# Kernel optimization log

Hardware: AMD Instinct MI355X
Metric: run time of the kernel (lower is better)

## Reference

```python
import math
import jax, jax.numpy as jnp
import numpy as np

# irreps layout (flat, e3nn ordering: all scalars first, then vectors as (mul,3)):
#   pseduo: 64x0e + 32x1o  -> dim 160, 96 irreps
#   edge:   32x0e + 32x1o  -> dim 128, 64 irreps
PS, PV = 64, 32
ES, EV = 32, 32
H, NB = 8, 16
N_NODES, N_EDGES = 8192, 65536
MSG_DIM = PS + 3 * PV           # msg_irreps = pseduo_irreps (default)
NIR = PS + PV                   # num_irreps of pseduo
SQRT3 = math.sqrt(3.0)

def _split(x, ns, nv):
    # flat spherical tensor -> (scalars [..,ns], vectors [..,nv,3])
    return x[..., :ns], x[..., ns:].reshape(x.shape[:-1] + (nv, 3))

def _o3_linear(s, v, Ws, Wv):
    # e3nn o3.Linear: independent channel mixing per l, fan-in normalized
    so = (s @ Ws) / math.sqrt(Ws.shape[0])
    vo = jnp.einsum('...ic,io->...oc', v, Wv) / math.sqrt(Wv.shape[0])
    return so, vo

def setup_inputs() -> dict:
    key = jax.random.key(0)
    k = jax.random.split(key, 20)
    f32 = jnp.float32
    return {
        'pseduo_x': jax.random.normal(k[0], (N_NODES, PS + 3 * PV), f32),
        'rbf': jax.random.normal(k[1], (N_EDGES, NB), f32),
        'rsh': jax.random.normal(k[2], (N_EDGES, ES + 3 * EV), f32),
        'edge_index': jax.random.randint(k[3], (2, N_EDGES), 0, N_NODES),
        'Wq_s': jax.random.normal(k[4], (PS, H * PS), f32),
        'Wq_v': jax.random.normal(k[5], (PV, H * PV), f32),
        'Wk_s': jax.random.normal(k[6], (2 * PS, H * PS), f32),
        'Wk_v': jax.random.normal(k[7], (2 * PV, H * PV), f32),
        'Wp_s': jax.random.normal(k[8], (2 * PS, ES), f32),
        'Wp_v': jax.random.normal(k[9], (2 * PV, EV), f32),
        'Wrbf': jax.random.normal(k[10], (NB, ES + EV), f32) / math.sqrt(NB),
        'Wv_s': jax.random.normal(k[11], (ES + EV, H * PS), f32),
        'Wv_v': jax.random.normal(k[12], (2 * EV, H * PV), f32),
        'Wm_s': jax.random.normal(k[13], (H * PS, PS), f32),
        'Wm_v': jax.random.normal(k[14], (H * PV, PV), f32),
        'ln_g': jnp.ones((NIR,), f32),
        'ln_b': jnp.zeros((NIR,), f32),
        'W1': jax.random.normal(k[15], (NIR, NIR), f32) / math.sqrt(NIR),
        'b1': jnp.zeros((NIR,), f32),
        'W2': jax.random.normal(k[16], (NIR, NIR), f32) / math.sqrt(NIR),
        'b2': jnp.zeros((NIR,), f32),
    }

def reference(pseduo_x, rbf, rsh, edge_index, Wq_s, Wq_v, Wk_s, Wk_v, Wp_s, Wp_v,
              Wrbf, Wv_s, Wv_v, Wm_s, Wm_v, ln_g, ln_b, W1, b1, W2, b2):
    src, dst = edge_index[0], edge_index[1]
    s, v = _split(pseduo_x, PS, PV)

    # pseduo_ij = cat([x_i, x_j]) -> irreps pseduo*2
    sij = jnp.concatenate([s[src], s[dst]], axis=-1)            # [E, 2*PS]
    vij = jnp.concatenate([v[src], v[dst]], axis=-2)            # [E, 2*PV, 3]

    # multi-head query (per node) and key (per edge)
    q_s, q_v = _o3_linear(s, v, Wq_s, Wq_v)
    q_s = q_s.reshape(-1, H, PS); q_v = q_v.reshape(-1, H, PV, 3)
    k_s, k_v = _o3_linear(sij, vij, Wk_s, Wk_v)
    k_s = k_s.reshape(-1, H, PS); k_v = k_v.reshape(-1, H, PV, 3)

    # edge filter: rsh_conv(rsh, rbf_lin(rbf))
    scal = rbf @ Wrbf                                           # [E, ES+EV]
    rs, rv = _split(rsh, ES, EV)
    e_s = rs * scal[:, :ES]
    e_v = rv * scal[:, ES:, None]

    # sph_ij = edge * pseduo_lin(pseduo_ij)   (elementwise on flat layout)
    p_s, p_v = _o3_linear(sij, vij, Wp_s, Wp_v)
    sph_s = e_s * p_s                                           # [E, ES]
    sph_v = e_v * p_v                                           # [E, EV, 3]

    # depthwise CG self-coupling x (x) x, filter {0e, 1o} -> 64x0e + 64x1o
    c0 = jnp.concatenate([sph_s * sph_s,
                          jnp.sum(sph_v * sph_v, axis=-1) / SQRT3], axis=-1)  # [E, 64]
    sv = sph_s[..., None] * sph_v                               # 0e x 1o -> 1o
    c1 = jnp.concatenate([sv, sv], axis=-2)                     # [E, 64, 3]

    val_s, val_v = _o3_linear(c0, c1, Wv_s, Wv_v)
    val_s = val_s.reshape(-1, H, PS); val_v = val_v.reshape(-1, H, PV, 3)

    # attention logits: (query[src] * key).sum over flat msg dim, per head
    proj = (jnp.einsum('ehd,ehd->eh', q_s[src], k_s) +
            jnp.einsum('ehdc,ehdc->eh', q_v[src], k_v))
    logits = proj / math.sqrt(MSG_DIM)

    # scatter-softmax over destination nodes
    m = jax.ops.segment_max(logits, dst, num_segments=N_NODES)
    ex = jnp.exp(logits - m[dst])
    den = jax.ops.segment_sum(ex, dst, num_segments=N_NODES)
    attn = ex / den[dst]                                        # [E, H]

    # scatter-aggregate messages to nodes
    msg_s = jax.ops.segment_sum(attn[..., None] * val_s, dst, num_segments=N_NODES)
    msg_v = jax.ops.segment_sum(attn[..., None, None] * val_v, dst, num_segments=N_NODES)

    m_s, m_v = _o3_linear(msg_s.reshape(-1, H * PS),
                          msg_v.reshape(-1, H * PV, 3), Wm_s, Wm_v)

    # NormGate: EvNorm (per-irrep norm, node LayerNorm) + 2-layer silu MLP gate
    n0 = jnp.concatenate([jnp.abs(m_s), jnp.linalg.norm(m_v, axis=-1)], axis=-1)  # [N, 96]
    mu = jnp.mean(n0, axis=-1, keepdims=True)
    var = jnp.var(n0, axis=-1, keepdims=True)
    x1 = (n0 - mu) / jnp.sqrt(var + 1e-5) * ln_g + ln_b
    inv = 1.0 / (n0 + 1e-6)                                    # 1 / (|h_l| + eps)
    g = jax.nn.silu(jax.nn.silu(x1 @ W1 + b1) @ W2 + b2)
    f = inv * g
    out_s = m_s * f[:, :PS]
    out_v = m_v * f[:, PS:, None]
    return jnp.concatenate([out_s, out_v.reshape(-1, 3 * PV)], axis=-1)
```

## Files before the change

kernel.cpp:

```cpp
#include <hip/hip_runtime.h>

typedef unsigned short u16;
typedef unsigned int u32;

#define NN 8192
#define NE 65536
#define INV160 0.07905694150420949f

__device__ __forceinline__ float BF(u16 u){ return __uint_as_float(((u32)u)<<16); }
__device__ __forceinline__ float LD(const void* p, u32 i, int f){
  return f ? ((const float*)p)[i] : BF(((const u16*)p)[i]);
}
__device__ __forceinline__ int LDI(const void* p, u32 i, int f64){
  return f64 ? (int)((const long long*)p)[i] : ((const int*)p)[i];
}

__global__ void k_detect(
    const void* b0, const void* b1, const void* b2, const void* b3,
    const void* b4, const void* b5, const void* b6, const void* b7,
    const void* b8, const void* b9, const void* b10, const void* b11,
    const void* b12, const void* b13, const void* b14, const void* b15,
    const void* b16, const void* b17, const void* b18, const void* b19,
    const void* b20, int* flags)
{
  const void* bufs[21] = {b0,b1,b2,b3,b4,b5,b6,b7,b8,b9,b10,
                          b11,b12,b13,b14,b15,b16,b17,b18,b19,b20};
  int i = threadIdx.x;
  if (i >= 21) return;
  const u32* w = (const u32*)bufs[i];
  if (i == 3){
    int allz = 1;
    for (int k=0;k<32;k++) if (w[2*k+1] != 0u) allz = 0;
    flags[3] = allz;
  } else {
    int cnt = 0;
    for (int k=0;k<40;k++){
      u32 lo = w[k] & 0xFFFFu;
      u32 e = (lo>>7)&0xFFu;
      if (e>=123u && e<=131u) cnt++;
    }
    flags[i] = (cnt>=20) ? 0 : 1;
  }
}

__global__ void k_sentinel(float* __restrict__ out, int n){
  int i = blockIdx.x*256+threadIdx.x;
  if (i<n) out[i] = 12345.0f;
}

__global__ __launch_bounds__(384) void k_prep4(
    const void* __restrict__ X, const void* __restrict__ Wq_s,
    const void* __restrict__ Wq_v, const void* __restrict__ Wk_s,
    const void* __restrict__ Wk_v, const int* __restrict__ flags,
    int hc0, float* __restrict__ qtab, float* __restrict__ kbtab,
    float* __restrict__ dotAA)
{
  __shared__ float xr[4][160];
  __shared__ float dsum[4][4];
  const int fX=flags[0], fqs=flags[4], fqv=flags[5], fks=flags[6], fkv=flags[7];
  const int fall = fqs & fqv & fks & fkv;
  const int t=threadIdx.x; const int n0=blockIdx.x*4;
  for(int u=t;u<640;u+=384){ int m=u/160,k=u-m*160; xr[m][k]=LD(X,(u32)(n0+m)*160+k,fX); }
  if (t<16) dsum[t>>2][t&3]=0.f;
  __syncthreads();
  if (t<256){
    const int o=hc0*64+t;
    float q[4]={0,0,0,0}, ka[4]={0,0,0,0}, kb[4]={0,0,0,0};
    if (fall){
      const float* wqs=(const float*)Wq_s;
      const float* wks=(const float*)Wk_s;
      for(int i=0;i<64;i++){
        float wq=wqs[(u32)i*512+o], wa=wks[(u32)i*512+o], wb=wks[(u32)(64+i)*512+o];
        #pragma unroll
        for(int m=0;m<4;m++){ float s=xr[m][i]; q[m]+=s*wq; ka[m]+=s*wa; kb[m]+=s*wb; }
      }
    } else {
      for(int i=0;i<64;i++){
        float wq=LD(Wq_s,(u32)i*512+o,fqs);
        float wa=LD(Wk_s,(u32)i*512+o,fks);
        float wb=LD(Wk_s,(u32)(64+i)*512+o,fks);
        #pragma unroll
        for(int m=0;m<4;m++){ float s=xr[m][i]; q[m]+=s*wq; ka[m]+=s*wa; kb[m]+=s*wb; }
      }
    }
    #pragma unroll
    for(int m=0;m<4;m++){
      float qs = q[m]*0.125f;
      float kas= ka[m]*0.08838834764831845f;
      float kbs= kb[m]*0.08838834764831845f;
      qtab [(u32)(n0+m)*640+t]=qs;
      kbtab[(u32)(n0+m)*640+t]=kbs;
      float d=qs*kas;
      for(int s2=1;s2<64;s2<<=1) d+=__shfl_xor(d,s2,64);
      if((t&63)==0) atomicAdd(&dsum[m][t>>6],d);
    }
  } else {
    const int ol=t-256;
    const int o=hc0*32+ol;
    float q[4][3]={}, ka[4][3]={}, kb[4][3]={};
    if (fall){
      const float* wqv=(const float*)Wq_v;
      const float* wkv=(const float*)Wk_v;
      for(int j=0;j<32;j++){
        float wq=wqv[(u32)j*256+o], wa=wkv[(u32)j*256+o], wb=wkv[(u32)(32+j)*256+o];
        #pragma unroll
        for(int m=0;m<4;m++){
          #pragma unroll
          for(int c=0;c<3;c++){
            float x=xr[m][64+j*3+c];
            q[m][c]+=x*wq; ka[m][c]+=x*wa; kb[m][c]+=x*wb;
          }
        }
      }
    } else {
      for(int j=0;j<32;j++){
        float wq=LD(Wq_v,(u32)j*256+o,fqv);
        float wa=LD(Wk_v,(u32)j*256+o,fkv);
        float wb=LD(Wk_v,(u32)(32+j)*256+o,fkv);
        #pragma unroll
        for(int m=0;m<4;m++){
          #pragma unroll
          for(int c=0;c<3;c++){
            float x=xr[m][64+j*3+c];
            q[m][c]+=x*wq; ka[m][c]+=x*wa; kb[m][c]+=x*wb;
          }
        }
      }
    }
    const float sq=0.17677669529663687f;
    const float sk=0.125f;
    #pragma unroll
    for(int m=0;m<4;m++){
      float d=0.f;
      u32 base=(u32)(n0+m)*640+256+(u32)ol*3;
      #pragma unroll
      for(int c=0;c<3;c++){
        float qs=q[m][c]*sq, kas=ka[m][c]*sk, kbs=kb[m][c]*sk;
        qtab[base+c]=qs; kbtab[base+c]=kbs;
        d+=qs*kas;
      }
      for(int s2=1;s2<32;s2<<=1) d+=__shfl_xor(d,s2,64);
      if((t&31)==0) atomicAdd(&dsum[m][ol>>5],d);
    }
  }
  __syncthreads();
  if (t<16){ int m=t>>2, hh=t&3; dotAA[(u32)(n0+m)*8+hc0+hh]=dsum[m][hh]; }
}

__global__ __launch_bounds__(512) void k_elog4(
    const void* __restrict__ ei, const int* __restrict__ flags,
    const float* __restrict__ qtab, const float* __restrict__ kbtab,
    const float* __restrict__ dotAA, const u32* __restrict__ elist,
    int hc0, float* __restrict__ logits)
{
  const int f64=flags[3];
  const int t=threadIdx.x;
  const int e=(int)elist[(u32)blockIdx.x*8+(t>>6)], l=t&63;
  const int src=LDI(ei,(u32)e,f64);
  const int dst=LDI(ei,(u32)NE+e,f64);
  const float4* q4=(const float4*)qtab + (u32)src*160;
  const float4* b4=(const float4*)kbtab + (u32)dst*160;
  float a0=0.f,a1=0.f,a2=0.f,a3=0.f;
  {
    float4 a=q4[l], b=b4[l];
    float d=a.x*b.x+a.y*b.y+a.z*b.z+a.w*b.w;
    int h=l>>4;
    a0+=(h==0)?d:0.f; a1+=(h==1)?d:0.f; a2+=(h==2)?d:0.f; a3+=(h==3)?d:0.f;
  }
  {
    float4 a=q4[64+l], b=b4[64+l];
    float d=a.x*b.x+a.y*b.y+a.z*b.z+a.w*b.w;
    int h=l/24;
    a0+=(h==0)?d:0.f; a1+=(h==1)?d:0.f; a2+=(h==2)?d:0.f;
  }
  if (l<32){
    float4 a=q4[128+l], b=b4[128+l];
    float d=a.x*b.x+a.y*b.y+a.z*b.z+a.w*b.w;
    a2+=(l<8)?d:0.f; a3+=(l>=8)?d:0.f;
  }
  for(int m=1;m<64;m<<=1){
    a0+=__shfl_xor(a0,m,64); a1+=__shfl_xor(a1,m,64);
    a2+=__shfl_xor(a2,m,64); a3+=__shfl_xor(a3,m,64);
  }
  if (l<4){
    float cr=(l==0)?a0:(l==1)?a1:(l==2)?a2:a3;
    logits[(u32)e*8+hc0+l]=(dotAA[(u32)src*8+hc0+l]+cr)*INV160;
  }
}

__global__ __launch_bounds__(256) void k_fold(
    const void* __restrict__ Wv_s, const void* __restrict__ Wv_v,
    const void* __restrict__ Wm_s, const void* __restrict__ Wm_v,
    const int* __restrict__ flags,
    float* __restrict__ Wfold, float* __restrict__ Vfold)
{
  const int fvs=flags[11], fvv=flags[12], fms=flags[13], fmv=flags[14];
  const int b=blockIdx.x, t=threadIdx.x;
  if (b<128){
    int idx=b*256+t;
    int i=idx>>6, o=idx&63;
    int h=i>>6, iin=i&63;
    float a=0.f;
    for(int d=0;d<64;d++)
      a += LD(Wv_s,(u32)iin*512 + h*64 + d, fvs) * LD(Wm_s,(u32)(h*64+d)*64 + o, fms);
    Wfold[idx]=a*0.0055242717280199026f;
  } else {
    int idx=(b-128)*256+t;
    int h=idx>>10, r=idx&1023, j2=r>>5, o2=r&31;
    float a=0.f;
    for(int dl=0;dl<32;dl++){
      int i2=h*32+dl;
      a += (LD(Wv_v,(u32)j2*256+i2,fvv)+LD(Wv_v,(u32)(32+j2)*256+i2,fvv))
           *LD(Wm_v,(u32)i2*32+o2,fmv);
    }
    Vfold[idx]=a*0.0078125f;
  }
}

__global__ __launch_bounds__(256) void k_pprep(
    const void* __restrict__ X, const void* __restrict__ Wp_s,
    const void* __restrict__ Wp_v, const int* __restrict__ flags,
    float* __restrict__ pA, float* __restrict__ pB)
{
  __shared__ float xr[160];
  const int fX=flags[0], fps=flags[8], fpv=flags[9];
  const int t=threadIdx.x, n=blockIdx.x;
  if (t<160) xr[t]=LD(X,(u32)n*160+t,fX);
  __syncthreads();
  if (t<64){
    const int j=t&31, half=t>>5;
    float a=0.f;
    if (fps){
      const float* wp=(const float*)Wp_s;
      for(int i=0;i<64;i++) a+=xr[i]*wp[(u32)(half*64+i)*32+j];
    } else {
      for(int i=0;i<64;i++) a+=xr[i]*LD(Wp_s,(u32)(half*64+i)*32+j,fps);
    }
    float* d_ = half? pB:pA;
    d_[(u32)n*128+j]=a*0.08838834764831845f;
  } else {
    const int idx=t-64;
    const int half=idx/96;
    const int r=idx-half*96;
    const int j=r/3, c=r-3*j;
    float a=0.f;
    if (fpv){
      const float* wp=(const float*)Wp_v;
      for(int k=0;k<32;k++) a+=xr[64+k*3+c]*wp[(u32)(half*32+k)*32+j];
    } else {
      for(int k=0;k<32;k++) a+=xr[64+k*3+c]*LD(Wp_v,(u32)(half*32+k)*32+j,fpv);
    }
    float* d_ = half? pB:pA;
    d_[(u32)n*128+32+j*3+c]=a*0.125f;
  }
}

__global__ __launch_bounds__(256) void k_count(
    const void* __restrict__ ei, const int* __restrict__ flags,
    u32* __restrict__ cnt)
{
  int e = blockIdx.x*256 + threadIdx.x;
  int dst = LDI(ei,(u32)NE+e,flags[3]);
  atomicAdd(&cnt[dst],1u);
}
__global__ __launch_bounds__(256) void k_scan(
    u32* __restrict__ cnt, u32* __restrict__ off, u32* __restrict__ cur)
{
  __shared__ u32 s[NN];
  __shared__ u32 tsum[256];
  const int t=threadIdx.x;
  for(int u=t;u<NN;u+=256) s[u]=cnt[u];
  __syncthreads();
  const u32 base=(u32)t*32;
  u32 sum=0;
  for(int k=0;k<32;k++) sum+=s[base+k];
  tsum[t]=sum;
  __syncthreads();
  if(t==0){
    u32 run=0;
    for(int i=0;i<256;i++){ u32 v=tsum[i]; tsum[i]=run; run+=v; }
  }
  __syncthreads();
  u32 run=tsum[t];
  for(int k=0;k<32;k++){
    u32 v=s[base+k];
    off[base+k]=run; cur[base+k]=run;
    run+=v;
  }
  if(t==255) off[NN]=run;
}
__global__ __launch_bounds__(256) void k_fill(
    const void* __restrict__ ei, const int* __restrict__ flags,
    u32* __restrict__ cur, u32* __restrict__ elist)
{
  int e = blockIdx.x*256 + threadIdx.x;
  int dst = LDI(ei,(u32)NE+e,flags[3]);
  u32 p = atomicAdd(&cur[dst],1u);
  elist[p] = (u32)e;
}

__global__ __launch_bounds__(256) void k_nodeval(
    const float* __restrict__ logits, const float* __restrict__ pA,
    const float* __restrict__ pBt,
    const u32* __restrict__ off, const u32* __restrict__ elist,
    const void* __restrict__ ei, const void* __restrict__ rbf,
    const void* __restrict__ rsh, const void* __restrict__ Wrbf,
    const float* __restrict__ Wfold, const float* __restrict__ Vfold,
    const void* __restrict__ ln_g, const void* __restrict__ ln_b,
    const void* __restrict__ W1, const void* __restrict__ b1,
    const void* __restrict__ W2, const void* __restrict__ b2,
    const int* __restrict__ flags, float* __restrict__ out)
{
  __shared__ float wrb[1024];
  __shared__ float pB[128];
  __shared__ float ubuf[8][160];
  __shared__ int   ebuf[8];
  __shared__ float ag[1280];
  __shared__ float partf[16][64];
  __shared__ float partv[192];
  __shared__ float mrow[160];
  __shared__ float n0[96], x1[96], y1[96], fl[96];
  const int frb=flags[1], frs=flags[2], f64=flags[3], fwr=flags[10];
  const int fg=flags[15], fbb=flags[16], f1=flags[17], fb1=flags[18];
  const int f2=flags[19], fb2=flags[20];
  const int fastg = frb & frs;
  const int fastt = fg & fbb & f1 & fb1 & f2 & fb2;
  const int t=threadIdx.x; const int n=blockIdx.x;
  for(int u=t;u<1024;u+=256) wrb[u]=LD(Wrbf,u,fwr);
  if (t<128) pB[t]=pBt[(u32)n*128+t];
  __syncthreads();

  const int h=t>>5, j=t&31;
  const u32 o0=off[n], o1=off[n+1];

  float mx=-3.4e38f;
  for(u32 p=o0+j; p<o1; p+=32) mx=fmaxf(mx, logits[(u32)elist[p]*8+h]);
  #pragma unroll
  for(int s2=1;s2<32;s2<<=1) mx=fmaxf(mx, __shfl_xor(mx,s2,64));
  float sm=0.f;
  for(u32 p=o0+j; p<o1; p+=32) sm+=__expf(logits[(u32)elist[p]*8+h]-mx);
  #pragma unroll
  for(int s2=1;s2<32;s2<<=1) sm+=__shfl_xor(sm,s2,64);
  const float winv=(sm>0.f)?1.f/sm:0.f;

  float a0=0.f,a1=0.f,a2=0.f,a3=0.f,a4=0.f;
  for (u32 base=o0; base<o1; base+=8){
    u32 rem=o1-base; int nb = rem<8u ? (int)rem : 8;
    if (h<nb){
      u32 e=elist[base+h];
      if (j==0) ebuf[h]=(int)e;
      int src=LDI(ei,e,f64);
      const float* pa=pA+(u32)src*128;
      float ps  = pa[j]        + pB[j];
      float pv0 = pa[32+j*3+0] + pB[32+j*3+0];
      float pv1 = pa[32+j*3+1] + pB[32+j*3+1];
      float pv2 = pa[32+j*3+2] + pB[32+j*3+2];
      float scs=0.f, scv=0.f;
      float rs0,rs1,rs2,rs3;
      if (fastg){
        const float* rb=(const float*)rbf + (size_t)e*16;
        #pragma unroll
        for(int r=0;r<16;r++){
          float x=rb[r];
          scs+=x*wrb[r*64+j]; scv+=x*wrb[r*64+32+j];
        }
        const float* rs=(const float*)rsh + (size_t)e*128;
        rs0=rs[j]; rs1=rs[32+j*3+0]; rs2=rs[32+j*3+1]; rs3=rs[32+j*3+2];
      } else {
        for(int r=0;r<16;r++){
          float x=LD(rbf,(u32)e*16+r,frb);
          scs+=x*wrb[r*64+j]; scv+=x*wrb[r*64+32+j];
        }
        rs0=LD(rsh,(u32)e*128+j,frs);
        rs1=LD(rsh,(u32)e*128+32+j*3+0,frs);
        rs2=LD(rsh,(u32)e*128+32+j*3+1,frs);
        rs3=LD(rsh,(u32)e*128+32+j*3+2,frs);
      }
      float ss = rs0 * scs * ps;
      float v0 = rs1 * scv * pv0;
      float v1 = rs2 * scv * pv1;
      float v2 = rs3 * scv * pv2;
      ubuf[h][j]        = ss*ss;
      ubuf[h][32+j]     = (v0*v0+v1*v1+v2*v2)*0.57735026918962576f;
      ubuf[h][64+3*j+0] = ss*v0;
      ubuf[h][64+3*j+1] = ss*v1;
      ubuf[h][64+3*j+2] = ss*v2;
    }
    __syncthreads();
    for(int q=0;q<nb;q++){
      float w=__expf(logits[(u32)ebuf[q]*8+h]-mx)*winv;
      a0+=w*ubuf[q][j];        a1+=w*ubuf[q][32+j];
      a2+=w*ubuf[q][64+3*j+0]; a3+=w*ubuf[q][64+3*j+1]; a4+=w*ubuf[q][64+3*j+2];
    }
    __syncthreads();
  }
  ag[h*64+j]=a0; ag[h*64+32+j]=a1;
  ag[512+h*96+3*j+0]=a2; ag[512+h*96+3*j+1]=a3; ag[512+h*96+3*j+2]=a4;
  __syncthreads();

  {
    const int o4=t&15, p=t>>4;
    const float4* Wf4=(const float4*)Wfold;
    float ax=0.f,ay=0.f,az=0.f,aw=0.f;
    const int i0=p*32;
    for(int i=i0;i<i0+32;i++){
      float a=ag[i];
      float4 wv=Wf4[(u32)i*16+o4];
      ax+=a*wv.x; ay+=a*wv.y; az+=a*wv.z; aw+=a*wv.w;
    }
    partf[p][o4*4+0]=ax; partf[p][o4*4+1]=ay;
    partf[p][o4*4+2]=az; partf[p][o4*4+3]=aw;
  }
  if (t<192){
    const int o2=t&31, c=(t>>5)%3, p=t/96;
    float a=0.f;
    for(int hh=p*4;hh<p*4+4;hh++)
      for(int j2=0;j2<32;j2++)
        a += ag[512+hh*96+j2*3+c]*Vfold[(u32)hh*1024+j2*32+o2];
    partv[t]=a;
  }
  __syncthreads();
  if (t<64){
    float s=0.f;
    #pragma unroll
    for(int p2=0;p2<16;p2++) s+=partf[p2][t];
    mrow[t]=s;
  } else if (t<160){
    int q=t-64;
    mrow[64+(q&31)*3+(q>>5)]=partv[q]+partv[q+96];
  }
  __syncthreads();

  if (t<96){
    float val;
    if (t<64) val=fabsf(mrow[t]);
    else { int o2=t-64;
      float a=mrow[64+o2*3],b=mrow[64+o2*3+1],c=mrow[64+o2*3+2];
      val=sqrtf(a*a+b*b+c*c); }
    n0[t]=val;
  }
  __syncthreads();
  float mu=0.f,ss2=0.f;
  for(int i=0;i<96;i++){ float v=n0[i]; mu+=v; ss2+=v*v; }
  mu*=(1.f/96.f);
  float var=fmaxf(ss2*(1.f/96.f)-mu*mu,0.f);
  float rstd=rsqrtf(var+1e-5f);
  if (t<96){
    float gv = fg  ? ((const float*)ln_g)[t] : LD(ln_g,t,fg);
    float bv = fbb ? ((const float*)ln_b)[t] : LD(ln_b,t,fbb);
    x1[t]=(n0[t]-mu)*rstd*gv+bv;
  }
  __syncthreads();
  if (t<96){
    float a = fb1 ? ((const float*)b1)[t] : LD(b1,t,fb1);
    if (fastt){
      const float* w1=(const float*)W1;
      for(int i=0;i<96;i++) a+=x1[i]*w1[(u32)i*96+t];
    } else {
      for(int i=0;i<96;i++) a+=x1[i]*LD(W1,i*96+t,f1);
    }
    y1[t]=a/(1.f+__expf(-a));
  }
  __syncthreads();
  if (t<96){
    float a = fb2 ? ((const float*)b2)[t] : LD(b2,t,fb2);
    if (fastt){
      const float* w2=(const float*)W2;
      for(int i=0;i<96;i++) a+=y1[i]*w2[(u32)i*96+t];
    } else {
      for(int i=0;i<96;i++) a+=y1[i]*LD(W2,i*96+t,f2);
    }
    float gg=a/(1.f+__expf(-a));
    fl[t]=gg/(n0[t]+1e-6f);
  }
  __syncthreads();
  if (t<160){
    float v;
    if (t<64) v=mrow[t]*fl[t];
    else { int q=t-64; int o2=q/3; v=mrow[t]*fl[64+o2]; }
    out[(u32)n*160+t]=v;
  }
}

extern "C" void kernel_launch(void* const* d_in, const int* in_sizes, int n_in,
                              void* d_out, int out_size, void* d_ws, size_t ws_size,
                              hipStream_t stream)
{
  (void)in_sizes; (void)n_in;
  const void* X    = d_in[0];
  const void* rbf  = d_in[1];
  const void* rsh  = d_in[2];
  const void* ei   = d_in[3];
  const void* Wq_s = d_in[4];
  const void* Wq_v = d_in[5];
  const void* Wk_s = d_in[6];
  const void* Wk_v = d_in[7];
  const void* Wp_s = d_in[8];
  const void* Wp_v = d_in[9];
  const void* Wrbf = d_in[10];
  const void* Wv_s = d_in[11];
  const void* Wv_v = d_in[12];
  const void* Wm_s = d_in[13];
  const void* Wm_v = d_in[14];
  const void* ln_g = d_in[15];
  const void* ln_b = d_in[16];
  const void* W1   = d_in[17];
  const void* b1   = d_in[18];
  const void* W2   = d_in[19];
  const void* b2   = d_in[20];

  char* w = (char*)d_ws;
  int* flags     = (int*)w;   w += 256;
  float* logits  = (float*)w; w += (size_t)NE*8*4;
  u32* imax      = (u32*)w;   w += (size_t)NN*8*4;
  float* den     = (float*)w; w += (size_t)NN*8*4;
  char* uni = w;              w += (size_t)NN*1280*4;
  float* qtab  = (float*)uni;
  float* kbtab = (float*)(uni + (size_t)NN*640*4);
  float* pA    = (float*)uni;
  float* pB    = (float*)(uni + (size_t)NN*128*4);
  u32* csr_off = imax;
  u32* csr_cur = imax + 12288;
  float* Wfold = (float*)((char*)imax + 98304);
  float* Vfold = (float*)((char*)imax + 229376);
  u32* elist   = (u32*)den;
  float* dotAA = (float*)d_out;
  size_t required = (size_t)(w - (char*)d_ws);

  if (ws_size < required){
    k_sentinel<<<(out_size+255)/256,256,0,stream>>>((float*)d_out, out_size);
    return;
  }

  k_detect<<<1,64,0,stream>>>(X,rbf,rsh,ei,Wq_s,Wq_v,Wk_s,Wk_v,Wp_s,Wp_v,
                              Wrbf,Wv_s,Wv_v,Wm_s,Wm_v,ln_g,ln_b,W1,b1,W2,b2,flags);
  k_fold<<<160,256,0,stream>>>(Wv_s,Wv_v,Wm_s,Wm_v,flags,Wfold,Vfold);
  hipMemsetAsync(imax, 0, (size_t)NN*4, stream);
  k_count<<<NE/256,256,0,stream>>>(ei,flags,imax);
  k_scan<<<1,256,0,stream>>>(imax,csr_off,csr_cur);
  k_fill<<<NE/256,256,0,stream>>>(ei,flags,csr_cur,elist);
  for (int c=0;c<2;c++){
    k_prep4<<<NN/4,384,0,stream>>>(X,Wq_s,Wq_v,Wk_s,Wk_v,flags,c*4,qtab,kbtab,dotAA);
    k_elog4<<<NE/8,512,0,stream>>>(ei,flags,qtab,kbtab,dotAA,elist,c*4,logits);
  }
  k_pprep<<<NN,256,0,stream>>>(X,Wp_s,Wp_v,flags,pA,pB);
  k_nodeval<<<NN,256,0,stream>>>(logits,pA,pB,csr_off,elist,ei,rbf,rsh,Wrbf,
                                 Wfold,Vfold,ln_g,ln_b,W1,b1,W2,b2,flags,(float*)d_out);
}
```

Measured before the change: 446.6 us.

## Process four nodes per block in k_nodeval to amortize weight reads

Result: faster. 428.6 us (-4.0%).

```diff
diff --git a/kernel.cpp b/kernel.cpp
--- a/kernel.cpp
+++ b/kernel.cpp
@@ -311,174 +311,224 @@
     const void* __restrict__ W2, const void* __restrict__ b2,
     const int* __restrict__ flags, float* __restrict__ out)
 {
-  __shared__ float wrb[1024];
-  __shared__ float pB[128];
-  __shared__ float ubuf[8][160];
+  __shared__ float ag[4][1280];
+  __shared__ float smemf[4096];
   __shared__ int   ebuf[8];
-  __shared__ float ag[1280];
-  __shared__ float partf[16][64];
-  __shared__ float partv[192];
-  __shared__ float mrow[160];
-  __shared__ float n0[96], x1[96], y1[96], fl[96];
+  float* wrb = smemf;
+  float (*pB4)[128]  = (float(*)[128])(smemf+1024);
+  float (*ubuf)[160] = (float(*)[160])(smemf+1536);
+  float (*partf)[4][64] = (float(*)[4][64])smemf;
+  float (*partv)[192] = (float(*)[192])(smemf+1024);
+  float (*mrow)[160]  = (float(*)[160])(smemf+1792);
+  float (*n0_)[96]    = (float(*)[96])(smemf+2432);
+  float (*x1_)[96]    = (float(*)[96])(smemf+2816);
+  float (*y1_)[96]    = (float(*)[96])(smemf+3200);
+  float (*fl_)[96]    = (float(*)[96])(smemf+3584);
+  float* stat = smemf+3968;
+
   const int frb=flags[1], frs=flags[2], f64=flags[3], fwr=flags[10];
   const int fg=flags[15], fbb=flags[16], f1=flags[17], fb1=flags[18];
   const int f2=flags[19], fb2=flags[20];
   const int fastg = frb & frs;
-  const int fastt = fg & fbb & f1 & fb1 & f2 & fb2;
-  const int t=threadIdx.x; const int n=blockIdx.x;
+  const int fastt = f1 & f2;
+  const int t=threadIdx.x; const int g4=blockIdx.x*4;
   for(int u=t;u<1024;u+=256) wrb[u]=LD(Wrbf,u,fwr);
-  if (t<128) pB[t]=pBt[(u32)n*128+t];
+  #pragma unroll
+  for(int m=0;m<4;m++) if (t<128) pB4[m][t]=pBt[(u32)(g4+m)*128+t];
   __syncthreads();
 
   const int h=t>>5, j=t&31;
-  const u32 o0=off[n], o1=off[n+1];
-
-  float mx=-3.4e38f;
-  for(u32 p=o0+j; p<o1; p+=32) mx=fmaxf(mx, logits[(u32)elist[p]*8+h]);
-  #pragma unroll
-  for(int s2=1;s2<32;s2<<=1) mx=fmaxf(mx, __shfl_xor(mx,s2,64));
-  float sm=0.f;
-  for(u32 p=o0+j; p<o1; p+=32) sm+=__expf(logits[(u32)elist[p]*8+h]-mx);
-  #pragma unroll
-  for(int s2=1;s2<32;s2<<=1) sm+=__shfl_xor(sm,s2,64);
-  const float winv=(sm>0.f)?1.f/sm:0.f;
-
-  float a0=0.f,a1=0.f,a2=0.f,a3=0.f,a4=0.f;
-  for (u32 base=o0; base<o1; base+=8){
-    u32 rem=o1-base; int nb = rem<8u ? (int)rem : 8;
-    if (h<nb){
-      u32 e=elist[base+h];
-      if (j==0) ebuf[h]=(int)e;
-      int src=LDI(ei,e,f64);
-      const float* pa=pA+(u32)src*128;
-      float ps  = pa[j]        + pB[j];
-      float pv0 = pa[32+j*3+0] + pB[32+j*3+0];
-      float pv1 = pa[32+j*3+1] + pB[32+j*3+1];
-      float pv2 = pa[32+j*3+2] + pB[32+j*3+2];
-      float scs=0.f, scv=0.f;
-      float rs0,rs1,rs2,rs3;
-      if (fastg){
-        const float* rb=(const float*)rbf + (size_t)e*16;
-        #pragma unroll
-        for(int r=0;r<16;r++){
-          float x=rb[r];
-          scs+=x*wrb[r*64+j]; scv+=x*wrb[r*64+32+j];
+
+  for (int m=0;m<4;m++){
+    const int n=g4+m;
+    const u32 o0=off[n], o1=off[n+1];
+    float mx=-3.4e38f;
+    for(u32 p=o0+j; p<o1; p+=32) mx=fmaxf(mx, logits[(u32)elist[p]*8+h]);
+    #pragma unroll
+    for(int s2=1;s2<32;s2<<=1) mx=fmaxf(mx, __shfl_xor(mx,s2,64));
+    float sm=0.f;
+    for(u32 p=o0+j; p<o1; p+=32) sm+=__expf(logits[(u32)elist[p]*8+h]-mx);
+    #pragma unroll
+    for(int s2=1;s2<32;s2<<=1) sm+=__shfl_xor(sm,s2,64);
+    const float winv=(sm>0.f)?1.f/sm:0.f;
+
+    float a0=0.f,a1=0.f,a2=0.f,a3=0.f,a4=0.f;
+    for (u32 base=o0; base<o1; base+=8){
+      u32 rem=o1-base; int nb = rem<8u ? (int)rem : 8;
+      if (h<nb){
+        u32 e=elist[base+h];
+        if (j==0) ebuf[h]=(int)e;
+        int src=LDI(ei,e,f64);
+        const float* pa=pA+(u32)src*128;
+        float ps  = pa[j]        + pB4[m][j];
+        float pv0 = pa[32+j*3+0] + pB4[m][32+j*3+0];
+        float pv1 = pa[32+j*3+1] + pB4[m][32+j*3+1];
+        float pv2 = pa[32+j*3+2] + pB4[m][32+j*3+2];
+        float scs=0.f, scv=0.f;
+        float rs0,rs1,rs2,rs3;
+        if (fastg){
+          const float* rb=(const float*)rbf + (size_t)e*16;
+          #pragma unroll
+          for(int r=0;r<16;r++){
+            float x=rb[r];
+            scs+=x*wrb[r*64+j]; scv+=x*wrb[r*64+32+j];
+          }
+          const float* rs=(const float*)rsh + (size_t)e*128;
+          rs0=rs[j]; rs1=rs[32+j*3+0]; rs2=rs[32+j*3+1]; rs3=rs[32+j*3+2];
+        } else {
+          for(int r=0;r<16;r++){
+            float x=LD(rbf,(u32)e*16+r,frb);
+            scs+=x*wrb[r*64+j]; scv+=x*wrb[r*64+32+j];
+          }
+          rs0=LD(rsh,(u32)e*128+j,frs);
+          rs1=LD(rsh,(u32)e*128+32+j*3+0,frs);
+          rs2=LD(rsh,(u32)e*128+32+j*3+1,frs);
+          rs3=LD(rsh,(u32)e*128+32+j*3+2,frs);
         }
-        const float* rs=(const float*)rsh + (size_t)e*128;
-        rs0=rs[j]; rs1=rs[32+j*3+0]; rs2=rs[32+j*3+1]; rs3=rs[32+j*3+2];
-      } else {
-        for(int r=0;r<16;r++){
-          float x=LD(rbf,(u32)e*16+r,frb);
-          scs+=x*wrb[r*64+j]; scv+=x*wrb[r*64+32+j];
-        }
-        rs0=LD(rsh,(u32)e*128+j,frs);
-        rs1=LD(rsh,(u32)e*128+32+j*3+0,frs);
-        rs2=LD(rsh,(u32)e*128+32+j*3+1,frs);
-        rs3=LD(rsh,(u32)e*128+32+j*3+2,frs);
-      }
-      float ss = rs0 * scs * ps;
-      float v0 = rs1 * scv * pv0;
-      float v1 = rs2 * scv * pv1;
-      float v2 = rs3 * scv * pv2;
-      ubuf[h][j]        = ss*ss;
-      ubuf[h][32+j]     = (v0*v0+v1*v1+v2*v2)*0.57735026918962576f;
-      ubuf[h][64+3*j+0] = ss*v0;
-      ubuf[h][64+3*j+1] = ss*v1;
-      ubuf[h][64+3*j+2] = ss*v2;
-    }
-    __syncthreads();
-    for(int q=0;q<nb;q++){
-      float w=__expf(logits[(u32)ebuf[q]*8+h]-mx)*winv;
-      a0+=w*ubuf[q][j];        a1+=w*ubuf[q][32+j];
-      a2+=w*ubuf[q][64+3*j+0]; a3+=w*ubuf[q][64+3*j+1]; a4+=w*ubuf[q][64+3*j+2];
-    }
-    __syncthreads();
-  }
-  ag[h*64+j]=a0; ag[h*64+32+j]=a1;
-  ag[512+h*96+3*j+0]=a2; ag[512+h*96+3*j+1]=a3; ag[512+h*96+3*j+2]=a4;
+        float ss = rs0 * scs * ps;
+        float v0 = rs1 * scv * pv0;
+        float v1 = rs2 * scv * pv1;
+        float v2 = rs3 * scv * pv2;
+        ubuf[h][j]        = ss*ss;
+        ubuf[h][32+j]     = (v0*v0+v1*v1+v2*v2)*0.57735026918962576f;
+        ubuf[h][64+3*j+0] = ss*v0;
+        ubuf[h][64+3*j+1] = ss*v1;
+        ubuf[h][64+3*j+2] = ss*v2;
+      }
+      __syncthreads();
+      for(int q=0;q<nb;q++){
+        float w=__expf(logits[(u32)ebuf[q]*8+h]-mx)*winv;
+        a0+=w*ubuf[q][j];        a1+=w*ubuf[q][32+j];
+        a2+=w*ubuf[q][64+3*j+0]; a3+=w*ubuf[q][64+3*j+1]; a4+=w*ubuf[q][64+3*j+2];
+      }
+      __syncthreads();
+    }
+    ag[m][h*64+j]=a0; ag[m][h*64+32+j]=a1;
+    ag[m][512+h*96+3*j+0]=a2; ag[m][512+h*96+3*j+1]=a3; ag[m][512+h*96+3*j+2]=a4;
+  }
   __syncthreads();
 
   {
-    const int o4=t&15, p=t>>4;
+    const int o4=t&15, pp=t>>4;
+    const int m=pp&3, gq=pp>>2;
     const float4* Wf4=(const float4*)Wfold;
     float ax=0.f,ay=0.f,az=0.f,aw=0.f;
-    const int i0=p*32;
-    for(int i=i0;i<i0+32;i++){
-      float a=ag[i];
+    const int i0=gq*128;
+    for(int i=i0;i<i0+128;i++){
+      float a=ag[m][i];
       float4 wv=Wf4[(u32)i*16+o4];
       ax+=a*wv.x; ay+=a*wv.y; az+=a*wv.z; aw+=a*wv.w;
     }
-    partf[p][o4*4+0]=ax; partf[p][o4*4+1]=ay;
-    partf[p][o4*4+2]=az; partf[p][o4*4+3]=aw;
+    partf[gq][m][o4*4+0]=ax; partf[gq][m][o4*4+1]=ay;
+    partf[gq][m][o4*4+2]=az; partf[gq][m][o4*4+3]=aw;
   }
   if (t<192){
     const int o2=t&31, c=(t>>5)%3, p=t/96;
-    float a=0.f;
+    float a[4]={0.f,0.f,0.f,0.f};
     for(int hh=p*4;hh<p*4+4;hh++)
-      for(int j2=0;j2<32;j2++)
-        a += ag[512+hh*96+j2*3+c]*Vfold[(u32)hh*1024+j2*32+o2];
-    partv[t]=a;
-  }
-  __syncthreads();
-  if (t<64){
-    float s=0.f;
-    #pragma unroll
-    for(int p2=0;p2<16;p2++) s+=partf[p2][t];
-    mrow[t]=s;
-  } else if (t<160){
-    int q=t-64;
-    mrow[64+(q&31)*3+(q>>5)]=partv[q]+partv[q+96];
-  }
-  __syncthreads();
-
+      for(int j2=0;j2<32;j2++){
+        float v=Vfold[(u32)hh*1024+j2*32+o2];
+        #pragma unroll
+        for(int m=0;m<4;m++) a[m]+=ag[m][512+hh*96+j2*3+c]*v;
+      }
+    #pragma unroll
+    for(int m=0;m<4;m++) partv[m][t]=a[m];
+  }
+  __syncthreads();
+  {
+    const int o=t&63, m=t>>6;
+    mrow[m][o]=partf[0][m][o]+partf[1][m][o]+partf[2][m][o]+partf[3][m][o];
+  }
   if (t<96){
-    float val;
-    if (t<64) val=fabsf(mrow[t]);
-    else { int o2=t-64;
-      float a=mrow[64+o2*3],b=mrow[64+o2*3+1],c=mrow[64+o2*3+2];
-      val=sqrtf(a*a+b*b+c*c); }
-    n0[t]=val;
-  }
-  __syncthreads();
-  float mu=0.f,ss2=0.f;
-  for(int i=0;i<96;i++){ float v=n0[i]; mu+=v; ss2+=v*v; }
-  mu*=(1.f/96.f);
-  float var=fmaxf(ss2*(1.f/96.f)-mu*mu,0.f);
-  float rstd=rsqrtf(var+1e-5f);
+    #pragma unroll
+    for(int m=0;m<4;m++)
+      mrow[m][64+(t&31)*3+(t>>5)]=partv[m][t]+partv[m][t+96];
+  }
+  __syncthreads();
+
+  if (t<96){
+    #pragma unroll
+    for(int m=0;m<4;m++){
+      float val;
+      if (t<64) val=fabsf(mrow[m][t]);
+      else { int o2=t-64;
+        float a=mrow[m][64+o2*3],b=mrow[m][64+o2*3+1],c=mrow[m][64+o2*3+2];
+        val=sqrtf(a*a+b*b+c*c); }
+      n0_[m][t]=val;
+    }
+  }
+  __syncthreads();
+  {
+    const int m=t>>6;
+    float mu=0.f,ss2=0.f;
+    for(int i=0;i<96;i++){ float v=n0_[m][i]; mu+=v; ss2+=v*v; }
+    mu*=(1.f/96.f);
+    float var=fmaxf(ss2*(1.f/96.f)-mu*mu,0.f);
+    float rstd=rsqrtf(var+1e-5f);
+    if ((t&63)==0){ stat[m]=mu; stat[4+m]=rstd; }
+  }
+  __syncthreads();
   if (t<96){
     float gv = fg  ? ((const float*)ln_g)[t] : LD(ln_g,t,fg);
     float bv = fbb ? ((const float*)ln_b)[t] : LD(ln_b,t,fbb);
-    x1[t]=(n0[t]-mu)*rstd*gv+bv;
+    #pragma unroll
+    for(int m=0;m<4;m++)
+      x1_[m][t]=(n0_[m][t]-stat[m])*stat[4+m]*gv+bv;
   }
   __syncthreads();
   if (t<96){
-    float a = fb1 ? ((const float*)b1)[t] : LD(b1,t,fb1);
+    float bb = fb1 ? ((const float*)b1)[t] : LD(b1,t,fb1);
+    float a[4]={bb,bb,bb,bb};
     if (fastt){
       const float* w1=(const float*)W1;
-      for(int i=0;i<96;i++) a+=x1[i]*w1[(u32)i*96+t];
+      for(int i=0;i<96;i++){
+        float w=w1[(u32)i*96+t];
+        #pragma unroll
+        for(int m=0;m<4;m++) a[m]+=x1_[m][i]*w;
+      }
     } else {
-      for(int i=0;i<96;i++) a+=x1[i]*LD(W1,i*96+t,f1);
-    }
-    y1[t]=a/(1.f+__expf(-a));
+      for(int i=0;i<96;i++){
+        float w=LD(W1,i*96+t,f1);
+        #pragma unroll
+        for(int m=0;m<4;m++) a[m]+=x1_[m][i]*w;
+      }
+    }
+    #pragma unroll
+    for(int m=0;m<4;m++) y1_[m][t]=a[m]/(1.f+__expf(-a[m]));
   }
   __syncthreads();
   if (t<96){
-    float a = fb2 ? ((const float*)b2)[t] : LD(b2,t,fb2);
+    float bb = fb2 ? ((const float*)b2)[t] : LD(b2,t,fb2);
+    float a[4]={bb,bb,bb,bb};
     if (fastt){
       const float* w2=(const float*)W2;
-      for(int i=0;i<96;i++) a+=y1[i]*w2[(u32)i*96+t];
+      for(int i=0;i<96;i++){
+        float w=w2[(u32)i*96+t];
+        #pragma unroll
+        for(int m=0;m<4;m++) a[m]+=y1_[m][i]*w;
+      }
     } else {
-      for(int i=0;i<96;i++) a+=y1[i]*LD(W2,i*96+t,f2);
-    }
-    float gg=a/(1.f+__expf(-a));
-    fl[t]=gg/(n0[t]+1e-6f);
+      for(int i=0;i<96;i++){
+        float w=LD(W2,i*96+t,f2);
+        #pragma unroll
+        for(int m=0;m<4;m++) a[m]+=y1_[m][i]*w;
+      }
+    }
+    #pragma unroll
+    for(int m=0;m<4;m++){
+      float gg=a[m]/(1.f+__expf(-a[m]));
+      fl_[m][t]=gg/(n0_[m][t]+1e-6f);
+    }
   }
   __syncthreads();
   if (t<160){
-    float v;
-    if (t<64) v=mrow[t]*fl[t];
-    else { int q=t-64; int o2=q/3; v=mrow[t]*fl[64+o2]; }
-    out[(u32)n*160+t]=v;
+    #pragma unroll
+    for(int m=0;m<4;m++){
+      float v;
+      if (t<64) v=mrow[m][t]*fl_[m][t];
+      else { int q=t-64; int o2=q/3; v=mrow[m][t]*fl_[m][64+o2]; }
+      out[(u32)(g4+m)*160+t]=v;
+    }
   }
 }
 
@@ -544,6 +594,6 @@
     k_elog4<<<NE/8,512,0,stream>>>(ei,flags,qtab,kbtab,dotAA,elist,c*4,logits);
   }
   k_pprep<<<NN,256,0,stream>>>(X,Wp_s,Wp_v,flags,pA,pB);
-  k_nodeval<<<NN,256,0,stream>>>(logits,pA,pB,csr_off,elist,ei,rbf,rsh,Wrbf,
-                                 Wfold,Vfold,ln_g,ln_b,W1,b1,W2,b2,flags,(float*)d_out);
-}
+  k_nodeval<<<NN/4,256,0,stream>>>(logits,pA,pB,csr_off,elist,ei,rbf,rsh,Wrbf,
+                                   Wfold,Vfold,ln_g,ln_b,W1,b1,W2,b2,flags,(float*)d_out);
+}
```
